# Kernel tuning notes

Measured on AMD Instinct MI355X. Metric: run time of the kernel, lower is better.

Reference implementation:

```python
import jax, jax.numpy as jnp
import numpy as np

D_IN, D_H, D_G, H, B = 512, 256, 128, 8, 4096
EPS_LN = 1e-6
EPS_STD = 1e-6


def setup_inputs() -> dict:
    key = jax.random.key(0)
    ks = jax.random.split(key, 4)
    x = jax.random.normal(ks[0], (B, D_IN), dtype=jnp.float32)
    # Dense params (flax kernel layout: (in, out)), lecun-normal-ish init
    Wh = jax.random.normal(ks[1], (D_IN, D_H), dtype=jnp.float32) / np.sqrt(D_IN)
    bh = jnp.zeros((D_H,), dtype=jnp.float32)
    Wz1 = jax.random.normal(ks[2], (D_IN, H * D_H), dtype=jnp.float32) / np.sqrt(D_IN)
    Wz2 = jax.random.normal(ks[3], (D_IN, H * D_G), dtype=jnp.float32) / np.sqrt(D_IN)
    ln_scale = jnp.ones((D_H,), dtype=jnp.float32)
    ln_bias = jnp.zeros((D_H,), dtype=jnp.float32)
    return {"x": x, "Wh": Wh, "bh": bh, "Wz1": Wz1, "Wz2": Wz2,
            "ln_scale": ln_scale, "ln_bias": ln_bias}


def _layer_norm(a, scale, bias):
    mu = jnp.mean(a, axis=-1, keepdims=True)
    var = jnp.var(a, axis=-1, keepdims=True)
    return (a - mu) * jax.lax.rsqrt(var + EPS_LN) * scale + bias


def reference(x, Wh, bh, Wz1, Wz2, ln_scale, ln_bias):
    sz_b = x.shape[0]
    # h: (B, d_h)
    h = _layer_norm(jax.nn.relu(x @ Wh + bh), ln_scale, ln_bias)
    z1 = (x @ Wz1).reshape(sz_b, H, D_H)   # (B, H, d_h)
    z2 = (x @ Wz2).reshape(sz_b, H, D_G)   # (B, H, d_g)
    # w = z2^T @ z1 over heads: (B, d_g, d_h)
    w = jnp.einsum('bhg,bhd->bgd', z2, z1)
    # per-row standardization (population std, ddof=0) + tanh
    mu = jnp.mean(w, axis=-1, keepdims=True)
    sd = jnp.std(w, axis=-1, keepdims=True)
    w = jnp.tanh((w - mu) / (sd + EPS_STD))
    # y = w @ h: (B, d_g)
    y = jnp.einsum('bgd,bd->bg', w, h)
    return h, y
```

## Files before the change

### kernel.cpp

```cpp
#include <hip/hip_runtime.h>
#include <hip/hip_bf16.h>
#include <cstdint>

#define BATCH 4096
#define DIN   512
#define DH    256
#define DG    128
#define NH    8
#define NTOT  3328
#define S1    264

typedef __bf16 bf16x8 __attribute__((ext_vector_type(8)));
typedef float  f32x4  __attribute__((ext_vector_type(4)));

__device__ __forceinline__ unsigned short f2bf(float f) {
    union { float f; uint32_t u; } v; v.f = f;
    uint32_t u = v.u;
    u += 0x7fffu + ((u >> 16) & 1u);
    return (unsigned short)(u >> 16);
}
__device__ __forceinline__ float bf2f(unsigned short s) {
    union { uint32_t u; float f; } v; v.u = ((uint32_t)s) << 16;
    return v.f;
}
__device__ __forceinline__ void bf8_to_f8(uint4 u, float4& a, float4& b) {
    a.x = bf2f((unsigned short)(u.x & 0xffff)); a.y = bf2f((unsigned short)(u.x >> 16));
    a.z = bf2f((unsigned short)(u.y & 0xffff)); a.w = bf2f((unsigned short)(u.y >> 16));
    b.x = bf2f((unsigned short)(u.z & 0xffff)); b.y = bf2f((unsigned short)(u.z >> 16));
    b.z = bf2f((unsigned short)(u.w & 0xffff)); b.w = bf2f((unsigned short)(u.w >> 16));
}

__device__ __forceinline__ void async16(const unsigned short* g, unsigned short* l) {
    __builtin_amdgcn_global_load_lds(
        (const __attribute__((address_space(1))) unsigned int*)(uintptr_t)g,
        (__attribute__((address_space(3))) unsigned int*)(uintptr_t)l,
        16, 0, 0);
}

__global__ __launch_bounds__(256) void prep_kernel(const float* __restrict__ x,
                                                   const float* __restrict__ Wh,
                                                   const float* __restrict__ Wz1,
                                                   const float* __restrict__ Wz2,
                                                   unsigned short* __restrict__ xb,
                                                   unsigned short* __restrict__ Wt) {
    __shared__ float tile[32][33];
    int bid = blockIdx.x;
    int t = threadIdx.x;
    if (bid < 2048) {
        int i = (bid * 256 + t) * 4;
        float4 v = *(const float4*)(x + i);
        ushort4 o;
        o.x = f2bf(v.x); o.y = f2bf(v.y); o.z = f2bf(v.z); o.w = f2bf(v.w);
        *(ushort4*)(xb + i) = o;
        return;
    }
    int b2 = bid - 2048;
    int n0 = (b2 % 104) * 32;
    int k0 = (b2 / 104) * 32;
    const float* W; int ldn, nl;
    if (n0 < 256)       { W = Wh;  ldn = 256;  nl = n0; }
    else if (n0 < 2304) { W = Wz1; ldn = 2048; nl = n0 - 256; }
    else                { W = Wz2; ldn = 1024; nl = n0 - 2304; }
    int tx = t & 31, ty = t >> 5;
    #pragma unroll
    for (int i = 0; i < 4; i++) {
        int kk = ty + i * 8;
        tile[kk][tx] = W[(size_t)(k0 + kk) * ldn + nl + tx];
    }
    __syncthreads();
    #pragma unroll
    for (int i = 0; i < 4; i++) {
        int nn = ty + i * 8;
        Wt[(size_t)(n0 + nn) * 512 + k0 + tx] = f2bf(tile[tx][nn]);
    }
}

__global__ __launch_bounds__(256) void gemm_kernel(const unsigned short* __restrict__ xb,
                                                   const unsigned short* __restrict__ Wt,
                                                   unsigned short* __restrict__ Zb) {
    __shared__ unsigned short As[128 * 64];
    __shared__ unsigned short Bs[128 * 64];
    const int m0 = blockIdx.y * 128;
    const int n0 = blockIdx.x * 128;
    const int t = threadIdx.x;
    const int w = t >> 6, lane = t & 63;
    const int wm = (w >> 1) * 64, wn = (w & 1) * 64;
    const int lrow = lane & 15, q = lane >> 4;

    f32x4 acc[4][4] = {};

    for (int k0 = 0; k0 < DIN; k0 += 64) {
        __syncthreads();
        #pragma unroll
        for (int j = 0; j < 4; j++) {
            int gidx = (w * 4 + j) * 64 + lane;
            int row = gidx >> 3, slot = gidx & 7;
            int src = slot ^ (row & 7);
            const unsigned short* ga = xb + (size_t)(m0 + row) * DIN + k0 + src * 8;
            const unsigned short* gb = Wt + (size_t)(n0 + row) * DIN + k0 + src * 8;
            async16(ga, As + (w * 4 + j) * 512);
            async16(gb, Bs + (w * 4 + j) * 512);
        }
        __syncthreads();
        #pragma unroll
        for (int ks = 0; ks < 2; ks++) {
            bf16x8 af[4], bfr[4];
            #pragma unroll
            for (int i = 0; i < 4; i++) {
                int row = wm + i * 16 + lrow;
                int phys = (ks * 4 + q) ^ (row & 7);
                af[i] = *reinterpret_cast<const bf16x8*>(As + row * 64 + phys * 8);
            }
            #pragma unroll
            for (int j = 0; j < 4; j++) {
                int row = wn + j * 16 + lrow;
                int phys = (ks * 4 + q) ^ (row & 7);
                bfr[j] = *reinterpret_cast<const bf16x8*>(Bs + row * 64 + phys * 8);
            }
            #pragma unroll
            for (int i = 0; i < 4; i++)
                #pragma unroll
                for (int j = 0; j < 4; j++)
                    acc[i][j] = __builtin_amdgcn_mfma_f32_16x16x32_bf16(af[i], bfr[j], acc[i][j], 0, 0, 0);
        }
    }
    #pragma unroll
    for (int i = 0; i < 4; i++)
        #pragma unroll
        for (int j = 0; j < 4; j++) {
            int col = n0 + wn + j * 16 + lrow;
            int rbase = m0 + wm + i * 16 + q * 4;
            #pragma unroll
            for (int r = 0; r < 4; r++)
                Zb[(size_t)(rbase + r) * NTOT + col] = f2bf(acc[i][j][r]);
        }
}

__global__ __launch_bounds__(256) void attn_kernel(const unsigned short* __restrict__ Zb,
                                                   const float* __restrict__ bh,
                                                   const float* __restrict__ lns,
                                                   const float* __restrict__ lnb,
                                                   float* __restrict__ h_out,
                                                   float* __restrict__ y_out) {
    __shared__ float z1s[9 * S1];
    __shared__ float z2s[NH * DG];
    __shared__ float hs[DH];
    __shared__ float GL[9][9];
    __shared__ unsigned short z1cb[DH * 8];
    __shared__ unsigned short z2A[DG * 8];
    __shared__ unsigned short zpad[8];
    __shared__ float red[4][3];
    const int b = blockIdx.x;
    const int t = threadIdx.x;
    const int wv = t >> 6, lane = t & 63;
    const unsigned short* Zrow = Zb + (size_t)b * NTOT;

    {
        uint4 v1 = *(const uint4*)(Zrow + 256 + t * 8);
        float4 a, c; bf8_to_f8(v1, a, c);
        int hh = t >> 5, d0 = (t & 31) * 8;
        *(float4*)(z1s + hh * S1 + d0)     = a;
        *(float4*)(z1s + hh * S1 + d0 + 4) = c;
        if (t < 128) {
            uint4 v2 = *(const uint4*)(Zrow + 2304 + t * 8);
            float4 e, f; bf8_to_f8(v2, e, f);
            *(float4*)(z2s + t * 8)     = e;
            *(float4*)(z2s + t * 8 + 4) = f;
        }
        z1s[8 * S1 + t] = 1.0f;
        if (t < 8) zpad[t] = 0;
    }
    float v = fmaxf(bf2f(Zrow[t]) + bh[t], 0.0f);
    float s = v, sq = v * v;
    #pragma unroll
    for (int m = 32; m >= 1; m >>= 1) {
        s  += __shfl_xor(s,  m, 64);
        sq += __shfl_xor(sq, m, 64);
    }
    if (lane == 0) { red[wv][0] = s; red[wv][1] = sq; }
    __syncthreads();
    s  = red[0][0] + red[1][0] + red[2][0] + red[3][0];
    sq = red[0][1] + red[1][1] + red[2][1] + red[3][1];
    float mu  = s * (1.0f / 256.0f);
    float var = sq * (1.0f / 256.0f) - mu * mu;
    float hval = (v - mu) * rsqrtf(var + 1e-6f) * lns[t] + lnb[t];
    hs[t] = hval;
    h_out[(size_t)b * DH + t] = hval;
    float hp = hval;
    #pragma unroll
    for (int m = 32; m >= 1; m >>= 1) hp += __shfl_xor(hp, m, 64);
    if (lane == 0) red[wv][2] = hp;

    #pragma unroll
    for (int j = 0; j < 11; j++) {
        int task = wv * 11 + j;
        int h = 0, rem = task;
        while (rem >= 9 - h) { rem -= 9 - h; h++; }
        int h2 = h + rem;
        float4 a = *(const float4*)(z1s + h  * S1 + lane * 4);
        float4 c = *(const float4*)(z1s + h2 * S1 + lane * 4);
        float p = a.x * c.x + a.y * c.y + a.z * c.z + a.w * c.w;
        #pragma unroll
        for (int m = 32; m >= 1; m >>= 1) p += __shfl_xor(p, m, 64);
        if (lane == 0) { GL[h][h2] = p; GL[h2][h] = p; }
    }
    __syncthreads();
    float Hsum = red[0][2] + red[1][2] + red[2][2] + red[3][2];

    {
        unsigned short pk[8];
        #pragma unroll
        for (int h = 0; h < NH; h++) {
            float c = z1s[h * S1 + t] - GL[h][8] * (1.0f / 256.0f);
            pk[h] = f2bf(c);
        }
        ushort4 lo = {pk[0], pk[1], pk[2], pk[3]};
        ushort4 hi = {pk[4], pk[5], pk[6], pk[7]};
        *(ushort4*)(z1cb + t * 8)     = lo;
        *(ushort4*)(z1cb + t * 8 + 4) = hi;
    }
    if (t < DG) {
        float z2g[NH];
        #pragma unroll
        for (int h = 0; h < NH; h++) z2g[h] = z2s[h * DG + t];
        float mug = 0.f, qg = 0.f;
        #pragma unroll
        for (int h = 0; h < NH; h++) {
            mug += z2g[h] * GL[h][8];
            float inn = 0.f;
            #pragma unroll
            for (int h2 = 0; h2 < NH; h2++) inn += z2g[h2] * GL[h][h2];
            qg += z2g[h] * inn;
        }
        mug *= (1.0f / 256.0f);
        qg  *= (1.0f / 256.0f);
        float vg = fmaxf(qg - mug * mug, 0.0f);
        float A = 2.0f * 1.4426950408889634f / (sqrtf(vg) + 1e-6f);
        unsigned short pk[8];
        #pragma unroll
        for (int h = 0; h < NH; h++) pk[h] = f2bf(z2g[h] * A);
        ushort4 lo = {pk[0], pk[1], pk[2], pk[3]};
        ushort4 hi = {pk[4], pk[5], pk[6], pk[7]};
        *(ushort4*)(z2A + t * 8)     = lo;
        *(ushort4*)(z2A + t * 8 + 4) = hi;
    }
    __syncthreads();

    const int lrow = lane & 15, q = lane >> 4;
    const unsigned short* bptr = (q == 0) ? (z1cb + lrow * 8) : zpad;
    const int binc = (q == 0) ? 128 : 0;
    bf16x8 af[2];
    #pragma unroll
    for (int gt = 0; gt < 2; gt++) {
        const unsigned short* aptr = (q == 0) ? (z2A + (wv * 32 + gt * 16 + lrow) * 8) : zpad;
        af[gt] = *reinterpret_cast<const bf16x8*>(aptr);
    }
    f32x4 czero = {};
    float yn[2][4] = {};
    #pragma unroll 4
    for (int dt = 0; dt < 16; dt++) {
        bf16x8 bfr = *reinterpret_cast<const bf16x8*>(bptr + dt * binc);
        float hv = hs[dt * 16 + lrow];
        #pragma unroll
        for (int gt = 0; gt < 2; gt++) {
            f32x4 c = __builtin_amdgcn_mfma_f32_16x16x32_bf16(af[gt], bfr, czero, 0, 0, 0);
            #pragma unroll
            for (int r = 0; r < 4; r++) {
                float e = __builtin_amdgcn_exp2f(c[r]);
                yn[gt][r] = fmaf(hv, __builtin_amdgcn_rcpf(e + 1.0f), yn[gt][r]);
            }
        }
    }
    #pragma unroll
    for (int m = 1; m <= 8; m <<= 1)
        #pragma unroll
        for (int gt = 0; gt < 2; gt++)
            #pragma unroll
            for (int r = 0; r < 4; r++)
                yn[gt][r] += __shfl_xor(yn[gt][r], m, 64);
    if (lrow == 0) {
        #pragma unroll
        for (int gt = 0; gt < 2; gt++)
            #pragma unroll
            for (int r = 0; r < 4; r++)
                y_out[(size_t)b * DG + wv * 32 + gt * 16 + q * 4 + r] = Hsum - 2.0f * yn[gt][r];
    }
}

extern "C" void kernel_launch(void* const* d_in, const int* in_sizes, int n_in,
                              void* d_out, int out_size, void* d_ws, size_t ws_size,
                              hipStream_t stream) {
    const float* x   = (const float*)d_in[0];
    const float* Wh  = (const float*)d_in[1];
    const float* bh  = (const float*)d_in[2];
    const float* Wz1 = (const float*)d_in[3];
    const float* Wz2 = (const float*)d_in[4];
    const float* lns = (const float*)d_in[5];
    const float* lnb = (const float*)d_in[6];
    float* h_out = (float*)d_out;
    float* y_out = h_out + (size_t)BATCH * DH;

    char* ws = (char*)d_ws;
    unsigned short* Zb = (unsigned short*)ws;
    unsigned short* xb = (unsigned short*)(ws + 27262976);
    unsigned short* Wt = (unsigned short*)(ws + 31457280);

    prep_kernel<<<3712, 256, 0, stream>>>(x, Wh, Wz1, Wz2, xb, Wt);
    gemm_kernel<<<dim3(NTOT / 128, BATCH / 128), 256, 0, stream>>>(xb, Wt, Zb);
    attn_kernel<<<BATCH, 256, 0, stream>>>(Zb, bh, lns, lnb, h_out, y_out);
}
```

Measured before the change: 151.6 us.

## Keep Z tiles in bf16 LDS and compute head Gram matrix with MFMA

The attention kernel now keeps z1/z2 in shared memory as raw bf16 instead of converting them to fp32. It computes the 9x9 head Gram matrix (including the ones-row for the means) with eight 16x16x32 bf16 MFMAs on a single wave. This replaces 44 wave-wide shuffle-reduced dot products and halves LDS footprint and stores. It also preloads the h values into registers before the main MFMA/tanh loop. Rows 9-15 of the MFMA input tile are left uninitialized, but their outputs are discarded.

New measurement: 144.1 us. -4.9%, faster.

```diff
diff --git a/kernel.cpp b/kernel.cpp
--- a/kernel.cpp
+++ b/kernel.cpp
@@ -8,7 +8,7 @@
 #define DG    128
 #define NH    8
 #define NTOT  3328
-#define S1    264
+#define S2    264
 
 typedef __bf16 bf16x8 __attribute__((ext_vector_type(8)));
 typedef float  f32x4  __attribute__((ext_vector_type(4)));
@@ -22,12 +22,6 @@
 __device__ __forceinline__ float bf2f(unsigned short s) {
     union { uint32_t u; float f; } v; v.u = ((uint32_t)s) << 16;
     return v.f;
-}
-__device__ __forceinline__ void bf8_to_f8(uint4 u, float4& a, float4& b) {
-    a.x = bf2f((unsigned short)(u.x & 0xffff)); a.y = bf2f((unsigned short)(u.x >> 16));
-    a.z = bf2f((unsigned short)(u.y & 0xffff)); a.w = bf2f((unsigned short)(u.y >> 16));
-    b.x = bf2f((unsigned short)(u.z & 0xffff)); b.y = bf2f((unsigned short)(u.z >> 16));
-    b.z = bf2f((unsigned short)(u.w & 0xffff)); b.w = bf2f((unsigned short)(u.w >> 16));
 }
 
 __device__ __forceinline__ void async16(const unsigned short* g, unsigned short* l) {
@@ -142,32 +136,28 @@
                                                    const float* __restrict__ lnb,
                                                    float* __restrict__ h_out,
                                                    float* __restrict__ y_out) {
-    __shared__ float z1s[9 * S1];
-    __shared__ float z2s[NH * DG];
-    __shared__ float hs[DH];
-    __shared__ float GL[9][9];
+    __shared__ unsigned short z1s[16 * S2];
+    __shared__ unsigned short z2s[NH * DG];
     __shared__ unsigned short z1cb[DH * 8];
     __shared__ unsigned short z2A[DG * 8];
     __shared__ unsigned short zpad[8];
+    __shared__ float hs[DH];
+    __shared__ float GL[9][9];
     __shared__ float red[4][3];
     const int b = blockIdx.x;
     const int t = threadIdx.x;
     const int wv = t >> 6, lane = t & 63;
+    const int lrow = lane & 15, q = lane >> 4;
     const unsigned short* Zrow = Zb + (size_t)b * NTOT;
 
     {
         uint4 v1 = *(const uint4*)(Zrow + 256 + t * 8);
-        float4 a, c; bf8_to_f8(v1, a, c);
-        int hh = t >> 5, d0 = (t & 31) * 8;
-        *(float4*)(z1s + hh * S1 + d0)     = a;
-        *(float4*)(z1s + hh * S1 + d0 + 4) = c;
+        *(uint4*)(z1s + (t >> 5) * S2 + (t & 31) * 8) = v1;
         if (t < 128) {
             uint4 v2 = *(const uint4*)(Zrow + 2304 + t * 8);
-            float4 e, f; bf8_to_f8(v2, e, f);
-            *(float4*)(z2s + t * 8)     = e;
-            *(float4*)(z2s + t * 8 + 4) = f;
-        }
-        z1s[8 * S1 + t] = 1.0f;
+            *(uint4*)(z2s + t * 8) = v2;
+        }
+        z1s[8 * S2 + t] = 0x3F80;
         if (t < 8) zpad[t] = 0;
     }
     float v = fmaxf(bf2f(Zrow[t]) + bh[t], 0.0f);
@@ -179,39 +169,40 @@
     }
     if (lane == 0) { red[wv][0] = s; red[wv][1] = sq; }
     __syncthreads();
-    s  = red[0][0] + red[1][0] + red[2][0] + red[3][0];
-    sq = red[0][1] + red[1][1] + red[2][1] + red[3][1];
-    float mu  = s * (1.0f / 256.0f);
-    float var = sq * (1.0f / 256.0f) - mu * mu;
-    float hval = (v - mu) * rsqrtf(var + 1e-6f) * lns[t] + lnb[t];
-    hs[t] = hval;
-    h_out[(size_t)b * DH + t] = hval;
-    float hp = hval;
-    #pragma unroll
-    for (int m = 32; m >= 1; m >>= 1) hp += __shfl_xor(hp, m, 64);
-    if (lane == 0) red[wv][2] = hp;
-
-    #pragma unroll
-    for (int j = 0; j < 11; j++) {
-        int task = wv * 11 + j;
-        int h = 0, rem = task;
-        while (rem >= 9 - h) { rem -= 9 - h; h++; }
-        int h2 = h + rem;
-        float4 a = *(const float4*)(z1s + h  * S1 + lane * 4);
-        float4 c = *(const float4*)(z1s + h2 * S1 + lane * 4);
-        float p = a.x * c.x + a.y * c.y + a.z * c.z + a.w * c.w;
-        #pragma unroll
-        for (int m = 32; m >= 1; m >>= 1) p += __shfl_xor(p, m, 64);
-        if (lane == 0) { GL[h][h2] = p; GL[h2][h] = p; }
+
+    if (wv == 3) {
+        f32x4 g = {};
+        #pragma unroll
+        for (int ks = 0; ks < 8; ks++) {
+            bf16x8 fr = *reinterpret_cast<const bf16x8*>(z1s + lrow * S2 + ks * 32 + q * 8);
+            g = __builtin_amdgcn_mfma_f32_16x16x32_bf16(fr, fr, g, 0, 0, 0);
+        }
+        #pragma unroll
+        for (int r = 0; r < 4; r++) {
+            int row = q * 4 + r;
+            if (row < 9 && lrow < 9) GL[row][lrow] = g[r];
+        }
+    }
+    {
+        float ss = red[0][0] + red[1][0] + red[2][0] + red[3][0];
+        float qq = red[0][1] + red[1][1] + red[2][1] + red[3][1];
+        float mu  = ss * (1.0f / 256.0f);
+        float var = qq * (1.0f / 256.0f) - mu * mu;
+        float hval = (v - mu) * rsqrtf(var + 1e-6f) * lns[t] + lnb[t];
+        hs[t] = hval;
+        h_out[(size_t)b * DH + t] = hval;
+        float hp = hval;
+        #pragma unroll
+        for (int m = 32; m >= 1; m >>= 1) hp += __shfl_xor(hp, m, 64);
+        if (lane == 0) red[wv][2] = hp;
     }
     __syncthreads();
-    float Hsum = red[0][2] + red[1][2] + red[2][2] + red[3][2];
 
     {
         unsigned short pk[8];
         #pragma unroll
         for (int h = 0; h < NH; h++) {
-            float c = z1s[h * S1 + t] - GL[h][8] * (1.0f / 256.0f);
+            float c = bf2f(z1s[h * S2 + t]) - GL[h][8] * (1.0f / 256.0f);
             pk[h] = f2bf(c);
         }
         ushort4 lo = {pk[0], pk[1], pk[2], pk[3]};
@@ -222,7 +213,7 @@
     if (t < DG) {
         float z2g[NH];
         #pragma unroll
-        for (int h = 0; h < NH; h++) z2g[h] = z2s[h * DG + t];
+        for (int h = 0; h < NH; h++) z2g[h] = bf2f(z2s[h * DG + t]);
         float mug = 0.f, qg = 0.f;
         #pragma unroll
         for (int h = 0; h < NH; h++) {
@@ -246,7 +237,6 @@
     }
     __syncthreads();
 
-    const int lrow = lane & 15, q = lane >> 4;
     const unsigned short* bptr = (q == 0) ? (z1cb + lrow * 8) : zpad;
     const int binc = (q == 0) ? 128 : 0;
     bf16x8 af[2];
@@ -255,19 +245,22 @@
         const unsigned short* aptr = (q == 0) ? (z2A + (wv * 32 + gt * 16 + lrow) * 8) : zpad;
         af[gt] = *reinterpret_cast<const bf16x8*>(aptr);
     }
+    float hv[16];
+    #pragma unroll
+    for (int dt = 0; dt < 16; dt++) hv[dt] = hs[dt * 16 + lrow];
+
     f32x4 czero = {};
     float yn[2][4] = {};
     #pragma unroll 4
     for (int dt = 0; dt < 16; dt++) {
         bf16x8 bfr = *reinterpret_cast<const bf16x8*>(bptr + dt * binc);
-        float hv = hs[dt * 16 + lrow];
         #pragma unroll
         for (int gt = 0; gt < 2; gt++) {
             f32x4 c = __builtin_amdgcn_mfma_f32_16x16x32_bf16(af[gt], bfr, czero, 0, 0, 0);
             #pragma unroll
             for (int r = 0; r < 4; r++) {
                 float e = __builtin_amdgcn_exp2f(c[r]);
-                yn[gt][r] = fmaf(hv, __builtin_amdgcn_rcpf(e + 1.0f), yn[gt][r]);
+                yn[gt][r] = fmaf(hv[dt], __builtin_amdgcn_rcpf(e + 1.0f), yn[gt][r]);
             }
         }
     }
@@ -279,6 +272,7 @@
             for (int r = 0; r < 4; r++)
                 yn[gt][r] += __shfl_xor(yn[gt][r], m, 64);
     if (lrow == 0) {
+        float Hsum = red[0][2] + red[1][2] + red[2][2] + red[3][2];
         #pragma unroll
         for (int gt = 0; gt < 2; gt++)
             #pragma unroll
```
